# Optimization experiments

Measured on AMD Instinct MI355X. Metric: run time of the kernel, lower is better.

Reference implementation:

```python
import jax, jax.numpy as jnp
import numpy as np

N_STATE = 1280
N_HEAD = 20
D_HEAD = N_STATE // N_HEAD  # 64
N_MLP = 4 * N_STATE         # 5120
EPS = 1e-5


def _layer_norm(x, gamma, beta):
    mu = jnp.mean(x, axis=-1, keepdims=True)
    var = jnp.mean(jnp.square(x - mu), axis=-1, keepdims=True)
    return (x - mu) * jax.lax.rsqrt(var + EPS) * gamma + beta


def setup_inputs() -> dict:
    key = jax.random.key(0)
    ks = jax.random.split(key, 16)
    s = lambda fan_in: 1.0 / np.sqrt(fan_in)
    d = {
        "x": jax.random.normal(ks[0], (1, 1500, N_STATE), jnp.float32),
        # attention projections (stored [in, out]; torch Linear does x @ W.T + b)
        "Wq": jax.random.normal(ks[1], (N_STATE, N_STATE), jnp.float32) * s(N_STATE),
        "bq": jax.random.normal(ks[2], (N_STATE,), jnp.float32) * 0.02,
        "Wk": jax.random.normal(ks[3], (N_STATE, N_STATE), jnp.float32) * s(N_STATE),  # no bias
        "Wv": jax.random.normal(ks[4], (N_STATE, N_STATE), jnp.float32) * s(N_STATE),
        "bv": jax.random.normal(ks[5], (N_STATE,), jnp.float32) * 0.02,
        "Wo": jax.random.normal(ks[6], (N_STATE, N_STATE), jnp.float32) * s(N_STATE),
        "bo": jax.random.normal(ks[7], (N_STATE,), jnp.float32) * 0.02,
        # layer norms
        "ln1_g": jnp.ones((N_STATE,), jnp.float32),
        "ln1_b": jnp.zeros((N_STATE,), jnp.float32),
        "ln2_g": jnp.ones((N_STATE,), jnp.float32),
        "ln2_b": jnp.zeros((N_STATE,), jnp.float32),
        # MLP
        "W1": jax.random.normal(ks[8], (N_STATE, N_MLP), jnp.float32) * s(N_STATE),
        "b1": jax.random.normal(ks[9], (N_MLP,), jnp.float32) * 0.02,
        "W2": jax.random.normal(ks[10], (N_MLP, N_STATE), jnp.float32) * s(N_MLP),
        "b2": jax.random.normal(ks[11], (N_STATE,), jnp.float32) * 0.02,
    }
    return d


def reference(x, Wq, bq, Wk, Wv, bv, Wo, bo, ln1_g, ln1_b, ln2_g, ln2_b, W1, b1, W2, b2):
    B, S, C = x.shape
    scale = D_HEAD ** -0.5

    # --- multi-head self-attention ---
    h = _layer_norm(x, ln1_g, ln1_b)
    q = (h @ Wq + bq).reshape(B, S, N_HEAD, D_HEAD)
    k = (h @ Wk).reshape(B, S, N_HEAD, D_HEAD)
    v = (h @ Wv + bv).reshape(B, S, N_HEAD, D_HEAD)
    # scores: [B, H, Q, K]; softmax over keys (dim=1 'k' in the torch einsum)
    scores = jnp.einsum('bqhd,bkhd->bhqk', q, k) * scale
    w = jax.nn.softmax(scores, axis=-1)
    attn = jnp.einsum('bhqk,bkhd->bqhd', w, v).reshape(B, S, C)
    attn = attn @ Wo + bo
    x = x + attn

    # --- MLP (exact GELU, matching torch nn.GELU default) ---
    h2 = _layer_norm(x, ln2_g, ln2_b)
    h2 = jax.nn.gelu(h2 @ W1 + b1, approximate=False)
    x = x + (h2 @ W2 + b2)
    return x
```

## Files before the change

kernel.cpp:

```cpp
#include <hip/hip_runtime.h>
#include <hip/hip_bf16.h>
#include <math.h>

typedef __bf16 bf16x8 __attribute__((ext_vector_type(8)));
typedef float f32x4 __attribute__((ext_vector_type(4)));

#define SEQ 1500
#define CDIM 1280
#define NHEAD 20
#define DHEAD 64
#define NMLP 5120
#define QKVN 3840
#define VTLD 1504
#define APAD 72

#define GLOAD_LDS16(gp, lp)                                                    \
  __builtin_amdgcn_global_load_lds(                                            \
      (const __attribute__((address_space(1))) unsigned int*)(gp),             \
      (__attribute__((address_space(3))) unsigned int*)(lp), 16, 0, 0)

__global__ void detect_kernel(const unsigned int* __restrict__ xw,
                              int* __restrict__ flag) {
  __shared__ int cnt[256];
  const unsigned int w = xw[threadIdx.x];
  const unsigned int e = (w >> 7) & 0xFF;
  cnt[threadIdx.x] = (e >= 100 && e <= 150) ? 1 : 0;
  __syncthreads();
  for (int s = 128; s > 0; s >>= 1) {
    if (threadIdx.x < (unsigned)s) cnt[threadIdx.x] += cnt[threadIdx.x + s];
    __syncthreads();
  }
  if (threadIdx.x == 0) flag[0] = (cnt[0] >= 160) ? 1 : 0;
}

__global__ __launch_bounds__(256) void convert_kernel(const void* __restrict__ src,
                                                      __bf16* __restrict__ dst,
                                                      int n, const int* __restrict__ flag) {
  const int isbf = flag[0];
  int i = blockIdx.x * 256 + threadIdx.x;
  const int stride = gridDim.x * 256;
  if (isbf) {
    const __bf16* s = (const __bf16*)src;
    for (; i < n; i += stride) dst[i] = s[i];
  } else {
    const float* s = (const float*)src;
    for (; i < n; i += stride) dst[i] = (__bf16)s[i];
  }
}

__global__ __launch_bounds__(256) void pack_params_kernel(
    const void* bq, const void* bv, const void* bo, const void* g1,
    const void* be1, const void* g2, const void* be2, const void* b1,
    const void* b2, __bf16* __restrict__ pb, const int* __restrict__ flag) {
  const int isbf = flag[0];
  const int i = blockIdx.x * 256 + threadIdx.x;
  if (i >= 16640) return;
  auto ld = [&](const void* p, int j) -> float {
    return isbf ? (float)((const __bf16*)p)[j] : ((const float*)p)[j];
  };
  float v;
  if (i < 3840) {
    if (i < 1280) v = ld(bq, i);
    else if (i < 2560) v = 0.f;
    else v = ld(bv, i - 2560);
  } else if (i < 5120) v = ld(bo, i - 3840);
  else if (i < 6400) v = ld(g1, i - 5120);
  else if (i < 7680) v = ld(be1, i - 6400);
  else if (i < 8960) v = ld(g2, i - 7680);
  else if (i < 10240) v = ld(be2, i - 8960);
  else if (i < 15360) v = ld(b1, i - 10240);
  else v = ld(b2, i - 15360);
  pb[i] = (__bf16)v;
}

__device__ __forceinline__ void transpose_body(const void* in, __bf16* out,
                                               int K, int N, int isbf) {
  __shared__ __bf16 t[32][33];
  const int tx = threadIdx.x, ty = threadIdx.y;
  const int n0 = blockIdx.x * 32, k0 = blockIdx.y * 32;
  if (isbf) {
    const __bf16* s = (const __bf16*)in;
#pragma unroll
    for (int i = ty; i < 32; i += 8)
      t[i][tx] = s[(size_t)(k0 + i) * N + n0 + tx];
  } else {
    const float* s = (const float*)in;
#pragma unroll
    for (int i = ty; i < 32; i += 8)
      t[i][tx] = (__bf16)s[(size_t)(k0 + i) * N + n0 + tx];
  }
  __syncthreads();
#pragma unroll
  for (int i = ty; i < 32; i += 8)
    out[(size_t)(n0 + i) * K + k0 + tx] = t[tx][i];
}

__global__ __launch_bounds__(256) void transpose_kernel(const void* __restrict__ in,
                                                        __bf16* __restrict__ out,
                                                        int K, int N,
                                                        const int* __restrict__ flag) {
  transpose_body(in, out, K, N, flag[0]);
}

__global__ __launch_bounds__(256) void transpose3_kernel(const void* __restrict__ Wq,
                                                         const void* __restrict__ Wk,
                                                         const void* __restrict__ Wv,
                                                         __bf16* __restrict__ out,
                                                         const int* __restrict__ flag) {
  const void* in = blockIdx.z == 0 ? Wq : (blockIdx.z == 1 ? Wk : Wv);
  transpose_body(in, out + (size_t)blockIdx.z * CDIM * CDIM, CDIM, CDIM, flag[0]);
}

__global__ __launch_bounds__(256) void transpose_act_kernel(const __bf16* __restrict__ in,
                                                            __bf16* __restrict__ out,
                                                            int istride) {
  __shared__ __bf16 t[32][33];
  const int tx = threadIdx.x, ty = threadIdx.y;
  const int n0 = blockIdx.x * 32, k0 = blockIdx.y * 32;
#pragma unroll
  for (int i = ty; i < 32; i += 8) {
    const int k = k0 + i;
    t[i][tx] = (k < SEQ) ? in[(size_t)k * istride + n0 + tx] : (__bf16)0.f;
  }
  __syncthreads();
#pragma unroll
  for (int i = ty; i < 32; i += 8) {
    const int kk = k0 + tx;
    if (kk < VTLD) out[(size_t)(n0 + i) * VTLD + kk] = t[tx][i];
  }
}

__global__ __launch_bounds__(256) void ln_kernel(const __bf16* __restrict__ X,
                                                 const __bf16* __restrict__ gamma,
                                                 const __bf16* __restrict__ beta,
                                                 __bf16* __restrict__ Y) {
  const int row = blockIdx.x;
  const __bf16* xr = X + (size_t)row * CDIM;
  float v[5];
  float s = 0.f, s2 = 0.f;
#pragma unroll
  for (int i = 0; i < 5; ++i) {
    v[i] = (float)xr[threadIdx.x + 256 * i];
    s += v[i];
    s2 += v[i] * v[i];
  }
  const int lane = threadIdx.x & 63, wv = threadIdx.x >> 6;
#pragma unroll
  for (int off = 32; off > 0; off >>= 1) {
    s += __shfl_down(s, off);
    s2 += __shfl_down(s2, off);
  }
  __shared__ float red[8];
  if (lane == 0) { red[wv] = s; red[4 + wv] = s2; }
  __syncthreads();
  s = red[0] + red[1] + red[2] + red[3];
  s2 = red[4] + red[5] + red[6] + red[7];
  const float mu = s * (1.f / CDIM);
  const float var = s2 * (1.f / CDIM) - mu * mu;
  const float rstd = rsqrtf(fmaxf(var, 0.f) + 1e-5f);
#pragma unroll
  for (int i = 0; i < 5; ++i) {
    const int c = threadIdx.x + 256 * i;
    Y[(size_t)row * CDIM + c] =
        (__bf16)((v[i] - mu) * rstd * (float)gamma[c] + (float)beta[c]);
  }
}

__global__ __launch_bounds__(256) void gemm64_kernel(
    const __bf16* __restrict__ A, const __bf16* __restrict__ Bt,
    const __bf16* __restrict__ bias, void* __restrict__ Cv,
    int M, int N, int K, int KS, int gelu, int nsplit) {
  __shared__ __bf16 As[64 * 32];
  __shared__ __bf16 Bs[128 * 32];
  const int bm = blockIdx.x, bn = blockIdx.y, sz = blockIdx.z;
  const int tid = threadIdx.x;
  const int lane = tid & 63, wave = tid >> 6;
  const int l16 = lane & 15, kq = (lane >> 4) << 3;
  const int lrow = lane >> 2, lcol = (lane & 3) << 3;
  const int wn = wave * 32;

  f32x4 acc[4][2];
  const f32x4 zero = {0.f, 0.f, 0.f, 0.f};
#pragma unroll
  for (int i = 0; i < 4; ++i)
#pragma unroll
    for (int j = 0; j < 2; ++j) acc[i][j] = zero;

  const int kbeg = sz * KS;
  int kend = kbeg + KS;
  if (kend > K) kend = K;

  for (int k0 = kbeg; k0 < kend; k0 += 32) {
    {
      int ga = bm * 64 + wave * 16 + lrow;
      if (ga > M - 1) ga = M - 1;
      GLOAD_LDS16(A + (size_t)ga * K + k0 + lcol, &As[wave * 16 * 32]);
    }
#pragma unroll
    for (int t = 0; t < 2; ++t) {
      const int seg = t * 4 + wave;
      const int gb = bn * 128 + seg * 16 + lrow;
      GLOAD_LDS16(Bt + (size_t)gb * K + k0 + lcol, &Bs[seg * 16 * 32]);
    }
    __syncthreads();
    bf16x8 af[4], bfr[2];
#pragma unroll
    for (int i = 0; i < 4; ++i)
      af[i] = *(const bf16x8*)(&As[(i * 16 + l16) * 32 + kq]);
#pragma unroll
    for (int j = 0; j < 2; ++j)
      bfr[j] = *(const bf16x8*)(&Bs[(wn + j * 16 + l16) * 32 + kq]);
#pragma unroll
    for (int i = 0; i < 4; ++i)
#pragma unroll
      for (int j = 0; j < 2; ++j)
        acc[i][j] = __builtin_amdgcn_mfma_f32_16x16x32_bf16(af[i], bfr[j],
                                                            acc[i][j], 0, 0, 0);
    __syncthreads();
  }

  const int rq4 = (lane >> 4) * 4;
  if (nsplit > 1) {
    float* P = (float*)Cv + (size_t)sz * M * N;
#pragma unroll
    for (int i = 0; i < 4; ++i)
#pragma unroll
      for (int r = 0; r < 4; ++r) {
        const int grow = bm * 64 + i * 16 + rq4 + r;
        if (grow >= M) continue;
#pragma unroll
        for (int j = 0; j < 2; ++j) {
          const int gcol = bn * 128 + wn + j * 16 + l16;
          P[(size_t)grow * N + gcol] = acc[i][j][r];
        }
      }
  } else {
    __bf16* Cb = (__bf16*)Cv;
#pragma unroll
    for (int i = 0; i < 4; ++i)
#pragma unroll
      for (int r = 0; r < 4; ++r) {
        const int grow = bm * 64 + i * 16 + rq4 + r;
        if (grow >= M) continue;
#pragma unroll
        for (int j = 0; j < 2; ++j) {
          const int gcol = bn * 128 + wn + j * 16 + l16;
          float vv = acc[i][j][r];
          if (bias) vv += (float)bias[gcol];
          if (gelu) vv = 0.5f * vv * (1.f + erff(vv * 0.70710678118654752f));
          Cb[(size_t)grow * N + gcol] = (__bf16)vv;
        }
      }
  }
}

__global__ __launch_bounds__(256) void reduce_kernel(
    const float* __restrict__ P, const __bf16* __restrict__ bias,
    const __bf16* __restrict__ resid, void* __restrict__ out,
    int MN, int N, int S, int useflag, const int* __restrict__ flag) {
  const int i = blockIdx.x * 256 + threadIdx.x;
  if (i >= MN) return;
  float v = 0.f;
  for (int s = 0; s < S; ++s) v += P[(size_t)s * MN + i];
  v += (float)bias[i % N];
  if (resid) v += (float)resid[i];
  const int outbf = useflag ? flag[0] : 1;
  if (outbf) ((__bf16*)out)[i] = (__bf16)v;
  else       ((float*)out)[i] = v;
}

__global__ __launch_bounds__(256) void attn_mfma_kernel(
    const __bf16* __restrict__ Q,
    const __bf16* __restrict__ Kk,
    const __bf16* __restrict__ Vt,
    __bf16* __restrict__ O,
    int rs) {
  const int h = blockIdx.y;
  const int q0 = blockIdx.x * 64;
  const int tid = threadIdx.x;
  const int wave = tid >> 6, lane = tid & 63;
  const int l16 = lane & 15, quad = lane >> 4;

  __shared__ __bf16 Ks[64 * APAD];
  __shared__ __bf16 Vs[64 * APAD];
  __shared__ __bf16 Ps[4][16 * APAD];

  bf16x8 qf[2];
  {
    int q = q0 + wave * 16 + l16;
    if (q > SEQ - 1) q = SEQ - 1;
    const __bf16* qp = Q + (size_t)q * rs + h * DHEAD + quad * 8;
    qf[0] = *(const bf16x8*)(qp);
    qf[1] = *(const bf16x8*)(qp + 32);
  }

  f32x4 oacc[4];
  const f32x4 zero = {0.f, 0.f, 0.f, 0.f};
#pragma unroll
  for (int jt = 0; jt < 4; ++jt) oacc[jt] = zero;
  float mrow[4], lrow[4];
#pragma unroll
  for (int r = 0; r < 4; ++r) { mrow[r] = -30000.f; lrow[r] = 0.f; }

  const int srow = tid >> 2;
  const int scol = (tid & 3) << 4;

  const __bf16* Kbase = Kk + h * DHEAD;
  const __bf16* Vbase = Vt + (size_t)(h * DHEAD + srow) * VTLD;

  for (int kt = 0; kt < 24; ++kt) {
    const int key0 = kt * 64;
    __syncthreads();
    {
      int gk = key0 + srow;
      if (gk > SEQ - 1) gk = SEQ - 1;
      const __bf16* kp = Kbase + (size_t)gk * rs + scol;
      *(bf16x8*)(&Ks[srow * APAD + scol]) = *(const bf16x8*)(kp);
      *(bf16x8*)(&Ks[srow * APAD + scol + 8]) = *(const bf16x8*)(kp + 8);
      const __bf16* vp = Vbase + key0 + scol;
      *(bf16x8*)(&Vs[srow * APAD + scol]) = *(const bf16x8*)(vp);
      *(bf16x8*)(&Vs[srow * APAD + scol + 8]) = *(const bf16x8*)(vp + 8);
    }
    __syncthreads();

    f32x4 s[4];
#pragma unroll
    for (int jt = 0; jt < 4; ++jt) s[jt] = zero;
#pragma unroll
    for (int jt = 0; jt < 4; ++jt)
#pragma unroll
      for (int ks = 0; ks < 2; ++ks) {
        const bf16x8 kf = *(const bf16x8*)(&Ks[(jt * 16 + l16) * APAD + ks * 32 + quad * 8]);
        s[jt] = __builtin_amdgcn_mfma_f32_16x16x32_bf16(qf[ks], kf, s[jt], 0, 0, 0);
      }

#pragma unroll
    for (int jt = 0; jt < 4; ++jt) {
      const int key = key0 + jt * 16 + l16;
#pragma unroll
      for (int r = 0; r < 4; ++r) {
        float sv = s[jt][r] * 0.125f;
        if (key >= SEQ) sv = -30000.f;
        s[jt][r] = sv;
      }
    }

#pragma unroll
    for (int r = 0; r < 4; ++r) {
      float tmax = fmaxf(fmaxf(s[0][r], s[1][r]), fmaxf(s[2][r], s[3][r]));
#pragma unroll
      for (int off = 8; off > 0; off >>= 1) tmax = fmaxf(tmax, __shfl_xor(tmax, off));
      const float mnew = fmaxf(mrow[r], tmax);
      const float alpha = __expf(mrow[r] - mnew);
      mrow[r] = mnew;
      lrow[r] *= alpha;
#pragma unroll
      for (int jt = 0; jt < 4; ++jt) oacc[jt][r] *= alpha;
#pragma unroll
      for (int jt = 0; jt < 4; ++jt) {
        const float p = __expf(s[jt][r] - mnew);
        lrow[r] += p;
        Ps[wave][(quad * 4 + r) * APAD + jt * 16 + l16] = (__bf16)p;
      }
    }
    __syncthreads();

    bf16x8 pf[2];
    pf[0] = *(const bf16x8*)(&Ps[wave][l16 * APAD + quad * 8]);
    pf[1] = *(const bf16x8*)(&Ps[wave][l16 * APAD + 32 + quad * 8]);
#pragma unroll
    for (int jt = 0; jt < 4; ++jt)
#pragma unroll
      for (int ks = 0; ks < 2; ++ks) {
        const bf16x8 vf = *(const bf16x8*)(&Vs[(jt * 16 + l16) * APAD + ks * 32 + quad * 8]);
        oacc[jt] = __builtin_amdgcn_mfma_f32_16x16x32_bf16(pf[ks], vf, oacc[jt], 0, 0, 0);
      }
  }

#pragma unroll
  for (int r = 0; r < 4; ++r) {
    float lt = lrow[r];
#pragma unroll
    for (int off = 8; off > 0; off >>= 1) lt += __shfl_xor(lt, off);
    const float inv = 1.f / lt;
    const int q = q0 + wave * 16 + quad * 4 + r;
    if (q < SEQ) {
#pragma unroll
      for (int jt = 0; jt < 4; ++jt)
        O[(size_t)q * CDIM + h * DHEAD + jt * 16 + l16] = (__bf16)(oacc[jt][r] * inv);
    }
  }
}

extern "C" void kernel_launch(void* const* d_in, const int* in_sizes, int n_in,
                              void* d_out, int out_size, void* d_ws, size_t ws_size,
                              hipStream_t stream) {
  const void* x   = d_in[0];
  const void* Wq  = d_in[1];
  const void* bq  = d_in[2];
  const void* Wk  = d_in[3];
  const void* Wv  = d_in[4];
  const void* bv  = d_in[5];
  const void* Wo  = d_in[6];
  const void* bo  = d_in[7];
  const void* g1  = d_in[8];
  const void* be1 = d_in[9];
  const void* g2  = d_in[10];
  const void* be2 = d_in[11];
  const void* W1  = d_in[12];
  const void* bm1 = d_in[13];
  const void* W2  = d_in[14];
  const void* bm2 = d_in[15];

  char* ws = (char*)d_ws;
  size_t off = 0;
  auto alloc = [&](size_t elems) {
    __bf16* p = (__bf16*)(ws + off);
    off += elems * sizeof(__bf16);
    return p;
  };
  __bf16* Wqkvt = alloc((size_t)QKVN * CDIM);
  __bf16* Wot   = alloc((size_t)CDIM * CDIM);
  __bf16* W1t   = alloc((size_t)CDIM * NMLP);
  __bf16* W2t   = alloc((size_t)CDIM * NMLP);
  __bf16* qkvb  = alloc((size_t)SEQ * QKVN);
  __bf16* hb    = alloc((size_t)SEQ * CDIM);
  __bf16* xb    = alloc((size_t)SEQ * CDIM);
  __bf16* mb    = alloc((size_t)SEQ * NMLP);
  __bf16* pb    = alloc(20480);
  off = (off + 15) & ~(size_t)15;
  float* pscr = (float*)(ws + off);
  off += (size_t)2 * SEQ * CDIM * sizeof(float);
  int* flag = (int*)(ws + off);

  __bf16* vtb  = mb;
  __bf16* x1b  = qkvb;
  __bf16* h2b  = qkvb + (size_t)SEQ * CDIM;

  __bf16* qkvbias = pb + 0;
  __bf16* bo_b  = pb + 3840;
  __bf16* g1_b  = pb + 5120;
  __bf16* be1_b = pb + 6400;
  __bf16* g2_b  = pb + 7680;
  __bf16* be2_b = pb + 8960;
  __bf16* b1_b  = pb + 10240;
  __bf16* b2_b  = pb + 15360;

  detect_kernel<<<1, 256, 0, stream>>>((const unsigned int*)x, flag);
  convert_kernel<<<960, 256, 0, stream>>>(x, xb, SEQ * CDIM, flag);
  pack_params_kernel<<<65, 256, 0, stream>>>(bq, bv, bo, g1, be1, g2, be2,
                                             bm1, bm2, pb, flag);

  const dim3 tb(32, 8);
  transpose3_kernel<<<dim3(40, 40, 3), tb, 0, stream>>>(Wq, Wk, Wv, Wqkvt, flag);
  transpose_kernel<<<dim3(40, 40), tb, 0, stream>>>(Wo, Wot, CDIM, CDIM, flag);
  transpose_kernel<<<dim3(160, 40), tb, 0, stream>>>(W1, W1t, CDIM, NMLP, flag);
  transpose_kernel<<<dim3(40, 160), tb, 0, stream>>>(W2, W2t, NMLP, CDIM, flag);

  ln_kernel<<<SEQ, 256, 0, stream>>>(xb, g1_b, be1_b, hb);
  gemm64_kernel<<<dim3(24, 30, 1), 256, 0, stream>>>(
      hb, Wqkvt, qkvbias, qkvb, SEQ, QKVN, CDIM, CDIM, 0, 1);
  transpose_act_kernel<<<dim3(40, 47), tb, 0, stream>>>(qkvb + 2560, vtb, QKVN);
  attn_mfma_kernel<<<dim3(24, NHEAD), 256, 0, stream>>>(
      qkvb, qkvb + 1280, vtb, hb, QKVN);
  gemm64_kernel<<<dim3(24, 10, 2), 256, 0, stream>>>(
      hb, Wot, nullptr, pscr, SEQ, CDIM, CDIM, 640, 0, 2);
  reduce_kernel<<<7500, 256, 0, stream>>>(pscr, bo_b, xb, x1b,
                                          SEQ * CDIM, CDIM, 2, 0, flag);
  ln_kernel<<<SEQ, 256, 0, stream>>>(x1b, g2_b, be2_b, h2b);
  gemm64_kernel<<<dim3(24, 40, 1), 256, 0, stream>>>(
      h2b, W1t, b1_b, mb, SEQ, NMLP, CDIM, CDIM, 1, 1);
  gemm64_kernel<<<dim3(24, 10, 2), 256, 0, stream>>>(
      mb, W2t, nullptr, pscr, SEQ, CDIM, NMLP, 2560, 0, 2);
  reduce_kernel<<<7500, 256, 0, stream>>>(pscr, b2_b, x1b, d_out,
                                          SEQ * CDIM, CDIM, 2, 1, flag);
}
```

Before: 411.4 us.

## Split attention over key halves, deepen GEMM K-step, drop input convert

Attention now splits the key range across two blocks per tile, writes unnormalised fp32 partials with per-row max and sum, and merges them in a new combine kernel, doubling the grid to improve CU occupancy. The GEMM main loop processes 64 of K per barrier pair using two LDS stages, halving synchronisation count. The fp32-to-bf16 input conversion kernel is removed by having layer norm and the residual reduce read the original input directly. The attention P-tile padding shrinks and one barrier is dropped, which risks a race on the per-wave P buffer; the combine pass adds extra fp32 traffic.

```diff
diff --git a/kernel.cpp b/kernel.cpp
--- a/kernel.cpp
+++ b/kernel.cpp
@@ -12,7 +12,7 @@
 #define NMLP 5120
 #define QKVN 3840
 #define VTLD 1504
-#define APAD 72
+#define APAD 68
 
 #define GLOAD_LDS16(gp, lp)                                                    \
   __builtin_amdgcn_global_load_lds(                                            \
@@ -31,21 +31,6 @@
     __syncthreads();
   }
   if (threadIdx.x == 0) flag[0] = (cnt[0] >= 160) ? 1 : 0;
-}
-
-__global__ __launch_bounds__(256) void convert_kernel(const void* __restrict__ src,
-                                                      __bf16* __restrict__ dst,
-                                                      int n, const int* __restrict__ flag) {
-  const int isbf = flag[0];
-  int i = blockIdx.x * 256 + threadIdx.x;
-  const int stride = gridDim.x * 256;
-  if (isbf) {
-    const __bf16* s = (const __bf16*)src;
-    for (; i < n; i += stride) dst[i] = s[i];
-  } else {
-    const float* s = (const float*)src;
-    for (; i < n; i += stride) dst[i] = (__bf16)s[i];
-  }
 }
 
 __global__ __launch_bounds__(256) void pack_params_kernel(
@@ -130,17 +115,20 @@
   }
 }
 
-__global__ __launch_bounds__(256) void ln_kernel(const __bf16* __restrict__ X,
+__global__ __launch_bounds__(256) void ln_kernel(const void* __restrict__ X,
                                                  const __bf16* __restrict__ gamma,
                                                  const __bf16* __restrict__ beta,
-                                                 __bf16* __restrict__ Y) {
+                                                 __bf16* __restrict__ Y,
+                                                 int xflag, const int* __restrict__ flag) {
+  const int isf32 = xflag ? (flag[0] == 0) : 0;
   const int row = blockIdx.x;
-  const __bf16* xr = X + (size_t)row * CDIM;
   float v[5];
   float s = 0.f, s2 = 0.f;
 #pragma unroll
   for (int i = 0; i < 5; ++i) {
-    v[i] = (float)xr[threadIdx.x + 256 * i];
+    const int c = threadIdx.x + 256 * i;
+    const size_t idx = (size_t)row * CDIM + c;
+    v[i] = isf32 ? ((const float*)X)[idx] : (float)((const __bf16*)X)[idx];
     s += v[i];
     s2 += v[i] * v[i];
   }
@@ -170,8 +158,8 @@
     const __bf16* __restrict__ A, const __bf16* __restrict__ Bt,
     const __bf16* __restrict__ bias, void* __restrict__ Cv,
     int M, int N, int K, int KS, int gelu, int nsplit) {
-  __shared__ __bf16 As[64 * 32];
-  __shared__ __bf16 Bs[128 * 32];
+  __shared__ __bf16 As[2][64 * 32];
+  __shared__ __bf16 Bs[2][128 * 32];
   const int bm = blockIdx.x, bn = blockIdx.y, sz = blockIdx.z;
   const int tid = threadIdx.x;
   const int lane = tid & 63, wave = tid >> 6;
@@ -190,32 +178,42 @@
   int kend = kbeg + KS;
   if (kend > K) kend = K;
 
-  for (int k0 = kbeg; k0 < kend; k0 += 32) {
-    {
-      int ga = bm * 64 + wave * 16 + lrow;
-      if (ga > M - 1) ga = M - 1;
-      GLOAD_LDS16(A + (size_t)ga * K + k0 + lcol, &As[wave * 16 * 32]);
-    }
-#pragma unroll
-    for (int t = 0; t < 2; ++t) {
-      const int seg = t * 4 + wave;
-      const int gb = bn * 128 + seg * 16 + lrow;
-      GLOAD_LDS16(Bt + (size_t)gb * K + k0 + lcol, &Bs[seg * 16 * 32]);
-    }
+  int ga = bm * 64 + wave * 16 + lrow;
+  if (ga > M - 1) ga = M - 1;
+  const __bf16* Ap = A + (size_t)ga * K + lcol;
+
+  for (int k0 = kbeg; k0 < kend; k0 += 64) {
+#pragma unroll
+    for (int c = 0; c < 2; ++c)
+      GLOAD_LDS16(Ap + k0 + c * 32, &As[c][wave * 512]);
+#pragma unroll
+    for (int c = 0; c < 2; ++c)
+#pragma unroll
+      for (int t = 0; t < 2; ++t) {
+        const int seg = t * 4 + wave;
+        const int gb = bn * 128 + seg * 16 + lrow;
+        GLOAD_LDS16(Bt + (size_t)gb * K + k0 + c * 32 + lcol, &Bs[c][seg * 512]);
+      }
     __syncthreads();
-    bf16x8 af[4], bfr[2];
+    bf16x8 af[4][2], bfr[2][2];
 #pragma unroll
     for (int i = 0; i < 4; ++i)
-      af[i] = *(const bf16x8*)(&As[(i * 16 + l16) * 32 + kq]);
+#pragma unroll
+      for (int c = 0; c < 2; ++c)
+        af[i][c] = *(const bf16x8*)(&As[c][(i * 16 + l16) * 32 + kq]);
 #pragma unroll
     for (int j = 0; j < 2; ++j)
-      bfr[j] = *(const bf16x8*)(&Bs[(wn + j * 16 + l16) * 32 + kq]);
+#pragma unroll
+      for (int c = 0; c < 2; ++c)
+        bfr[j][c] = *(const bf16x8*)(&Bs[c][(wn + j * 16 + l16) * 32 + kq]);
 #pragma unroll
     for (int i = 0; i < 4; ++i)
 #pragma unroll
       for (int j = 0; j < 2; ++j)
-        acc[i][j] = __builtin_amdgcn_mfma_f32_16x16x32_bf16(af[i], bfr[j],
-                                                            acc[i][j], 0, 0, 0);
+#pragma unroll
+        for (int c = 0; c < 2; ++c)
+          acc[i][j] = __builtin_amdgcn_mfma_f32_16x16x32_bf16(af[i][c], bfr[j][c],
+                                                              acc[i][j], 0, 0, 0);
     __syncthreads();
   }
 
@@ -256,15 +254,19 @@
 
 __global__ __launch_bounds__(256) void reduce_kernel(
     const float* __restrict__ P, const __bf16* __restrict__ bias,
-    const __bf16* __restrict__ resid, void* __restrict__ out,
-    int MN, int N, int S, int useflag, const int* __restrict__ flag) {
+    const void* __restrict__ resid, void* __restrict__ out,
+    int MN, int N, int S, int residflagged, int outflagged,
+    const int* __restrict__ flag) {
   const int i = blockIdx.x * 256 + threadIdx.x;
   if (i >= MN) return;
   float v = 0.f;
   for (int s = 0; s < S; ++s) v += P[(size_t)s * MN + i];
   v += (float)bias[i % N];
-  if (resid) v += (float)resid[i];
-  const int outbf = useflag ? flag[0] : 1;
+  if (resid) {
+    const int rf32 = residflagged ? (flag[0] == 0) : 0;
+    v += rf32 ? ((const float*)resid)[i] : (float)((const __bf16*)resid)[i];
+  }
+  const int outbf = outflagged ? flag[0] : 1;
   if (outbf) ((__bf16*)out)[i] = (__bf16)v;
   else       ((float*)out)[i] = v;
 }
@@ -273,10 +275,12 @@
     const __bf16* __restrict__ Q,
     const __bf16* __restrict__ Kk,
     const __bf16* __restrict__ Vt,
-    __bf16* __restrict__ O,
+    float* __restrict__ Opart,
+    float* __restrict__ ml,
     int rs) {
   const int h = blockIdx.y;
   const int q0 = blockIdx.x * 64;
+  const int z = blockIdx.z;
   const int tid = threadIdx.x;
   const int wave = tid >> 6, lane = tid & 63;
   const int l16 = lane & 15, quad = lane >> 4;
@@ -308,7 +312,7 @@
   const __bf16* Kbase = Kk + h * DHEAD;
   const __bf16* Vbase = Vt + (size_t)(h * DHEAD + srow) * VTLD;
 
-  for (int kt = 0; kt < 24; ++kt) {
+  for (int kt = z * 12; kt < z * 12 + 12; ++kt) {
     const int key0 = kt * 64;
     __syncthreads();
     {
@@ -363,7 +367,6 @@
         Ps[wave][(quad * 4 + r) * APAD + jt * 16 + l16] = (__bf16)p;
       }
     }
-    __syncthreads();
 
     bf16x8 pf[2];
     pf[0] = *(const bf16x8*)(&Ps[wave][l16 * APAD + quad * 8]);
@@ -377,19 +380,42 @@
       }
   }
 
+  float* Oz = Opart + (size_t)z * SEQ * CDIM;
 #pragma unroll
   for (int r = 0; r < 4; ++r) {
     float lt = lrow[r];
 #pragma unroll
     for (int off = 8; off > 0; off >>= 1) lt += __shfl_xor(lt, off);
-    const float inv = 1.f / lt;
     const int q = q0 + wave * 16 + quad * 4 + r;
     if (q < SEQ) {
 #pragma unroll
       for (int jt = 0; jt < 4; ++jt)
-        O[(size_t)q * CDIM + h * DHEAD + jt * 16 + l16] = (__bf16)(oacc[jt][r] * inv);
+        Oz[(size_t)q * CDIM + h * DHEAD + jt * 16 + l16] = oacc[jt][r];
+      if (l16 == 0) {
+        const size_t mi = ((size_t)(z * NHEAD + h) * SEQ + q) * 2;
+        ml[mi] = mrow[r];
+        ml[mi + 1] = lt;
+      }
     }
   }
+}
+
+__global__ __launch_bounds__(256) void attn_combine_kernel(
+    const float* __restrict__ Op, const float* __restrict__ ml,
+    __bf16* __restrict__ O) {
+  const int i = blockIdx.x * 256 + threadIdx.x;
+  if (i >= SEQ * CDIM) return;
+  const int q = i / CDIM;
+  const int h = (i % CDIM) >> 6;
+  const size_t m1i = ((size_t)h * SEQ + q) * 2;
+  const size_t m2i = ((size_t)(NHEAD + h) * SEQ + q) * 2;
+  const float m1 = ml[m1i], l1 = ml[m1i + 1];
+  const float m2 = ml[m2i], l2 = ml[m2i + 1];
+  const float M = fmaxf(m1, m2);
+  const float e1 = __expf(m1 - M), e2 = __expf(m2 - M);
+  const float v = (e1 * Op[i] + e2 * Op[(size_t)SEQ * CDIM + i]) /
+                  (e1 * l1 + e2 * l2);
+  O[i] = (__bf16)v;
 }
 
 extern "C" void kernel_launch(void* const* d_in, const int* in_sizes, int n_in,
@@ -425,12 +451,13 @@
   __bf16* W2t   = alloc((size_t)CDIM * NMLP);
   __bf16* qkvb  = alloc((size_t)SEQ * QKVN);
   __bf16* hb    = alloc((size_t)SEQ * CDIM);
-  __bf16* xb    = alloc((size_t)SEQ * CDIM);
   __bf16* mb    = alloc((size_t)SEQ * NMLP);
   __bf16* pb    = alloc(20480);
   off = (off + 15) & ~(size_t)15;
   float* pscr = (float*)(ws + off);
   off += (size_t)2 * SEQ * CDIM * sizeof(float);
+  float* mlb = (float*)(ws + off);
+  off += (size_t)2 * NHEAD * SEQ * 2 * sizeof(float);
   int* flag = (int*)(ws + off);
 
   __bf16* vtb  = mb;
@@ -447,7 +474,6 @@
   __bf16* b2_b  = pb + 15360;
 
   detect_kernel<<<1, 256, 0, stream>>>((const unsigned int*)x, flag);
-  convert_kernel<<<960, 256, 0, stream>>>(x, xb, SEQ * CDIM, flag);
   pack_params_kernel<<<65, 256, 0, stream>>>(bq, bv, bo, g1, be1, g2, be2,
                                              bm1, bm2, pb, flag);
 
@@ -457,21 +483,22 @@
   transpose_kernel<<<dim3(160, 40), tb, 0, stream>>>(W1, W1t, CDIM, NMLP, flag);
   transpose_kernel<<<dim3(40, 160), tb, 0, stream>>>(W2, W2t, NMLP, CDIM, flag);
 
-  ln_kernel<<<SEQ, 256, 0, stream>>>(xb, g1_b, be1_b, hb);
+  ln_kernel<<<SEQ, 256, 0, stream>>>(x, g1_b, be1_b, hb, 1, flag);
   gemm64_kernel<<<dim3(24, 30, 1), 256, 0, stream>>>(
       hb, Wqkvt, qkvbias, qkvb, SEQ, QKVN, CDIM, CDIM, 0, 1);
   transpose_act_kernel<<<dim3(40, 47), tb, 0, stream>>>(qkvb + 2560, vtb, QKVN);
-  attn_mfma_kernel<<<dim3(24, NHEAD), 256, 0, stream>>>(
-      qkvb, qkvb + 1280, vtb, hb, QKVN);
+  attn_mfma_kernel<<<dim3(24, NHEAD, 2), 256, 0, stream>>>(
+      qkvb, qkvb + 1280, vtb, pscr, mlb, QKVN);
+  attn_combine_kernel<<<7500, 256, 0, stream>>>(pscr, mlb, hb);
   gemm64_kernel<<<dim3(24, 10, 2), 256, 0, stream>>>(
       hb, Wot, nullptr, pscr, SEQ, CDIM, CDIM, 640, 0, 2);
-  reduce_kernel<<<7500, 256, 0, stream>>>(pscr, bo_b, xb, x1b,
-                                          SEQ * CDIM, CDIM, 2, 0, flag);
-  ln_kernel<<<SEQ, 256, 0, stream>>>(x1b, g2_b, be2_b, h2b);
+  reduce_kernel<<<7500, 256, 0, stream>>>(pscr, bo_b, x, x1b,
+                                          SEQ * CDIM, CDIM, 2, 1, 0, flag);
+  ln_kernel<<<SEQ, 256, 0, stream>>>(x1b, g2_b, be2_b, h2b, 0, flag);
   gemm64_kernel<<<dim3(24, 40, 1), 256, 0, stream>>>(
       h2b, W1t, b1_b, mb, SEQ, NMLP, CDIM, CDIM, 1, 1);
   gemm64_kernel<<<dim3(24, 10, 2), 256, 0, stream>>>(
       mb, W2t, nullptr, pscr, SEQ, CDIM, NMLP, 2560, 0, 2);
   reduce_kernel<<<7500, 256, 0, stream>>>(pscr, b2_b, x1b, d_out,
-                                          SEQ * CDIM, CDIM, 2, 1, flag);
-}
+                                          SEQ * CDIM, CDIM, 2, 0, 1, flag);
+}
```

Result: faster. 377.2 us (-8.3%).
